# Kernel tuning notes

Hardware: AMD Instinct MI355X
Metric: run time of the kernel (lower is better)

## Reference

```python
import jax, jax.numpy as jnp
import numpy as np

B, S, H, E, K, NH = 2, 2048, 1024, 8, 2, 8
HD = H // NH          # head dim = 128
HQ = H // 4           # seasonal encoder width = 256
CAP = int(B * S * 1.5 * K / E)  # expert capacity = 1536


def setup_inputs() -> dict:
    key = jax.random.key(0)
    ks = iter(jax.random.split(key, 32))

    def lin(shape):
        fan_in = shape[0]
        return jax.random.normal(next(ks), shape, jnp.float32) / np.sqrt(fan_in)

    inp = {
        "hidden_states": jax.random.normal(next(ks), (B, S, H), jnp.float32),
        # position embedding table [sequence_length, H]
        "pos_emb": jax.random.normal(next(ks), (S, H), jnp.float32) * 0.02,
        # temporal_encoder: Linear(H+2,H) -> ReLU -> Linear(H,H)
        "We1": lin((H + 2, H)), "be1": jnp.zeros((H,), jnp.float32),
        "We2": lin((H, H)),     "be2": jnp.zeros((H,), jnp.float32),
        # seasonal_encoder: Linear(1,H//4) -> ReLU -> Linear(H//4,H//4)
        "Ws1": lin((1, HQ)),   "bs1": jnp.zeros((HQ,), jnp.float32),
        "Ws2": lin((HQ, HQ)),  "bs2": jnp.zeros((HQ,), jnp.float32),
        # temporal_attention (MultiheadAttention, 8 heads)
        "Wq": lin((H, H)), "bq": jnp.zeros((H,), jnp.float32),
        "Wk": lin((H, H)), "bk": jnp.zeros((H,), jnp.float32),
        "Wv": lin((H, H)), "bv": jnp.zeros((H,), jnp.float32),
        "Wo": lin((H, H)), "bo": jnp.zeros((H,), jnp.float32),
        # temporal_router: Linear(H,H) -> ReLU -> Linear(H,E)
        "Wr1": lin((H, H)), "br1": jnp.zeros((H,), jnp.float32),
        "Wr2": lin((H, E)), "br2": jnp.zeros((E,), jnp.float32),
    }
    return inp


def _forward(hidden_states, pos_emb, We1, be1, We2, be2, Ws1, bs1, Ws2, bs2,
             Wq, bq, Wk, bk, Wv, bv, Wo, bo, Wr1, br1, Wr2, br2):
    b, s, h = hidden_states.shape
    # time features (time_info is None -> defaults)
    t = jnp.arange(s, dtype=jnp.float32)                   # [S]
    season = jnp.sin(t * 2.0 * jnp.pi / 24.0)              # [S]
    time_feat = jnp.broadcast_to(jnp.stack([t, season], -1), (b, s, 2))

    combined = jnp.concatenate([hidden_states, time_feat], axis=-1)  # [B,S,H+2]
    enc = jax.nn.relu(combined @ We1 + be1) @ We2 + be2              # [B,S,H]

    pos = pos_emb[:s]                                                # [S,H]
    seas = jax.nn.relu(season[:, None] @ Ws1 + bs1) @ Ws2 + bs2      # [S,H//4]
    seas_full = jnp.tile(seas, (1, h // seas.shape[-1]))             # [S,H] (expand to H)

    x = enc + pos[None] + seas_full[None]                            # [B,S,H]

    # self-attention (eval mode, no dropout)
    def heads(y):
        return y.reshape(b, s, NH, HD)
    q = heads(x @ Wq + bq)
    k = heads(x @ Wk + bk)
    v = heads(x @ Wv + bv)
    scores = jnp.einsum('bqhd,bkhd->bhqk', q, k) / np.sqrt(HD)
    attn = jax.nn.softmax(scores, axis=-1)
    ctx = jnp.einsum('bhqk,bkhd->bqhd', attn, v).reshape(b, s, h)
    x = ctx @ Wo + bo

    logits = jax.nn.relu(x @ Wr1 + br1) @ Wr2 + br2                  # [B,S,E]
    probs = jax.nn.softmax(logits, axis=-1)

    topv, topi = jax.lax.top_k(probs, K)                             # [B,S,K]
    topv = topv / topv.sum(-1, keepdims=True)

    onehot = jax.nn.one_hot(topi, E, dtype=probs.dtype)              # [B,S,K,E]
    disp0 = onehot.sum(-2)                                           # [B,S,E] (0/1)
    comb0 = (topv[..., None] * onehot).sum(-2)                       # [B,S,E]

    # only capacity slot 0 is ever written (per original code)
    dispatch = jnp.zeros((b, s, E, CAP), probs.dtype).at[..., 0].set(disp0)
    combine = jnp.zeros((b, s, E, CAP), probs.dtype).at[..., 0].set(comb0)

    p_mean = probs.mean(axis=(0, 1))                                 # [E]
    aux_loss = jnp.sum(p_mean * jnp.log(p_mean * E + 1e-9))
    return dispatch, combine, probs, aux_loss


def reference(hidden_states, pos_emb, We1, be1, We2, be2, Ws1, bs1, Ws2, bs2,
              Wq, bq, Wk, bk, Wv, bv, Wo, bo, Wr1, br1, Wr2, br2):
    return _forward(hidden_states, pos_emb, We1, be1, We2, be2, Ws1, bs1, Ws2, bs2,
                    Wq, bq, Wk, bk, Wv, bv, Wo, bo, Wr1, br1, Wr2, br2)
```

## Files before the change

kernel.cpp:

```cpp
#include <hip/hip_runtime.h>
#include <hip/hip_fp16.h>
#include <math.h>

#define N_TOK 4096
#define S_LEN 2048
#define H_DIM 1024
#define E_EXP 8
#define CAPV  1536
#define NHEAD 8
#define HDHD  128

typedef __attribute__((ext_vector_type(8))) _Float16 v8h;
typedef __attribute__((ext_vector_type(4))) float v4f;

__device__ __forceinline__ void splitf16(float v, unsigned short& h, unsigned short& l) {
    __half hh = __float2half(v);
    h = __half_as_ushort(hh);
    l = __half_as_ushort(__float2half(v - __half2float(hh)));
}

__device__ __forceinline__ void gld_lds16(const void* g, void* l) {
    __builtin_amdgcn_global_load_lds(
        (const __attribute__((address_space(1))) unsigned int*)g,
        (__attribute__((address_space(3))) unsigned int*)l,
        16, 0, 0);
}

__global__ void season_k(float* seasons) {
    int s = blockIdx.x * 256 + threadIdx.x;
    if (s < S_LEN) {
        double a = (double)s * 2.0 * M_PI / 24.0;
        seasons[s] = (float)sin(a);
    }
}

__global__ void seas24_k(const float* __restrict__ seasons,
                         const float* __restrict__ Ws1, const float* __restrict__ bs1,
                         const float* __restrict__ Ws2, const float* __restrict__ bs2,
                         float* __restrict__ seas24) {
    __shared__ float hbuf[256];
    int m = blockIdx.x;
    float sv = seasons[m];
    int j = threadIdx.x;
    hbuf[j] = fmaxf(sv * Ws1[j] + bs1[j], 0.f);
    __syncthreads();
    float acc = bs2[j];
    for (int i = 0; i < 256; ++i) acc = fmaf(hbuf[i], Ws2[i * 256 + j], acc);
    seas24[m * 256 + j] = acc;
}

__global__ void convert_split_k(const float* __restrict__ in,
                                unsigned short* __restrict__ hi,
                                unsigned short* __restrict__ lo, int n4) {
    int i = blockIdx.x * 256 + threadIdx.x;
    if (i >= n4) return;
    float4 v = ((const float4*)in)[i];
    ushort4 h, l;
    splitf16(v.x, h.x, l.x);
    splitf16(v.y, h.y, l.y);
    splitf16(v.z, h.z, l.z);
    splitf16(v.w, h.w, l.w);
    ((ushort4*)hi)[i] = h;
    ((ushort4*)lo)[i] = l;
}

__global__ __launch_bounds__(256) void wconv_t_k(const float* __restrict__ W,
                                                 unsigned short* __restrict__ Thi,
                                                 unsigned short* __restrict__ Tlo) {
    __shared__ unsigned short Hs[64][65];
    __shared__ unsigned short Ls[64][65];
    int k0 = blockIdx.y * 64, n0 = blockIdx.x * 64;
    int tid = threadIdx.x;
#pragma unroll
    for (int i = 0; i < 4; ++i) {
        int idx = tid + i * 256;
        int kk = idx >> 4, n4 = idx & 15;
        float4 v = *(const float4*)(W + (size_t)(k0 + kk) * 1024 + n0 + n4 * 4);
        unsigned short h, l;
        splitf16(v.x, h, l); Hs[n4 * 4 + 0][kk] = h; Ls[n4 * 4 + 0][kk] = l;
        splitf16(v.y, h, l); Hs[n4 * 4 + 1][kk] = h; Ls[n4 * 4 + 1][kk] = l;
        splitf16(v.z, h, l); Hs[n4 * 4 + 2][kk] = h; Ls[n4 * 4 + 2][kk] = l;
        splitf16(v.w, h, l); Hs[n4 * 4 + 3][kk] = h; Ls[n4 * 4 + 3][kk] = l;
    }
    __syncthreads();
#pragma unroll
    for (int i = 0; i < 4; ++i) {
        int idx = tid + i * 256;
        int n = idx >> 4, k4 = idx & 15;
        ushort4 h = make_ushort4(Hs[n][k4 * 4], Hs[n][k4 * 4 + 1], Hs[n][k4 * 4 + 2], Hs[n][k4 * 4 + 3]);
        ushort4 l = make_ushort4(Ls[n][k4 * 4], Ls[n][k4 * 4 + 1], Ls[n][k4 * 4 + 2], Ls[n][k4 * 4 + 3]);
        *(ushort4*)(Thi + (size_t)(n0 + n) * 1024 + k0 + k4 * 4) = h;
        *(ushort4*)(Tlo + (size_t)(n0 + n) * 1024 + k0 + k4 * 4) = l;
    }
}

template <int MODE, int EMITF, int EMITS, int EMITT>
__global__ __launch_bounds__(256, 2) void gemm_split(
    const unsigned short* __restrict__ Ahi, const unsigned short* __restrict__ Alo,
    const unsigned short* __restrict__ WThi, const unsigned short* __restrict__ WTlo,
    const float* __restrict__ bias, float* __restrict__ Cf,
    unsigned short* __restrict__ Chi, unsigned short* __restrict__ Clo,
    const float* __restrict__ rowT, const float* __restrict__ rowS,
    const float* __restrict__ seasons, const float* __restrict__ pos,
    const float* __restrict__ seas24, float escale) {
    __shared__ unsigned short Ash[128 * 32];
    __shared__ unsigned short Asl[128 * 32];
    __shared__ unsigned short Bsh[64 * 32];
    __shared__ unsigned short Bsl[64 * 32];
    int tid = threadIdx.x;
    int lane = tid & 63, w = tid >> 6;
    int l15 = lane & 15, l16 = lane >> 4;
    int wm = (w >> 1) * 64, wn = (w & 1) * 32;
    int m0 = blockIdx.y * 128, n0 = blockIdx.x * 64;

    int ac0 = w * 128 + lane;
    int ac1 = ac0 + 64;
    int bc  = w * 64 + lane;
    int ar0 = ac0 >> 2, ar1 = ac1 >> 2, bn = bc >> 2;
    size_t a_src0 = (size_t)(m0 + ar0) * 1024 + (((ac0 & 3) ^ (ar0 & 3)) * 8);
    size_t a_src1 = (size_t)(m0 + ar1) * 1024 + (((ac1 & 3) ^ (ar1 & 3)) * 8);
    size_t b_src  = (size_t)(n0 + bn) * 1024 + (((bc & 3) ^ (bn & 3)) * 8);
    unsigned short* ah_lds0 = &Ash[ac0 * 8];
    unsigned short* ah_lds1 = &Ash[ac1 * 8];
    unsigned short* al_lds0 = &Asl[ac0 * 8];
    unsigned short* al_lds1 = &Asl[ac1 * 8];
    unsigned short* bh_lds  = &Bsh[bc * 8];
    unsigned short* bl_lds  = &Bsl[bc * 8];

    int a_off[4], b_off[2];
#pragma unroll
    for (int mi = 0; mi < 4; ++mi) {
        int row = wm + mi * 16 + l15;
        a_off[mi] = row * 32 + ((l16 ^ (row & 3)) * 8);
    }
#pragma unroll
    for (int ni = 0; ni < 2; ++ni) {
        int n = wn + ni * 16 + l15;
        b_off[ni] = n * 32 + ((l16 ^ (n & 3)) * 8);
    }

    v4f acc[4][2] = {};

    for (int k0 = 0; k0 < 1024; k0 += 32) {
        __syncthreads();
        gld_lds16(Ahi + a_src0 + k0, ah_lds0);
        gld_lds16(Ahi + a_src1 + k0, ah_lds1);
        gld_lds16(Alo + a_src0 + k0, al_lds0);
        gld_lds16(Alo + a_src1 + k0, al_lds1);
        gld_lds16(WThi + b_src + k0, bh_lds);
        gld_lds16(WTlo + b_src + k0, bl_lds);
        __syncthreads();
        v8h ah[4], al[4], bh[2], bl[2];
#pragma unroll
        for (int mi = 0; mi < 4; ++mi) {
            ah[mi] = *(const v8h*)&Ash[a_off[mi]];
            al[mi] = *(const v8h*)&Asl[a_off[mi]];
        }
#pragma unroll
        for (int ni = 0; ni < 2; ++ni) {
            bh[ni] = *(const v8h*)&Bsh[b_off[ni]];
            bl[ni] = *(const v8h*)&Bsl[b_off[ni]];
        }
#pragma unroll
        for (int mi = 0; mi < 4; ++mi)
#pragma unroll
            for (int ni = 0; ni < 2; ++ni) {
                acc[mi][ni] = __builtin_amdgcn_mfma_f32_16x16x32_f16(ah[mi], bh[ni], acc[mi][ni], 0, 0, 0);
                acc[mi][ni] = __builtin_amdgcn_mfma_f32_16x16x32_f16(al[mi], bh[ni], acc[mi][ni], 0, 0, 0);
                acc[mi][ni] = __builtin_amdgcn_mfma_f32_16x16x32_f16(ah[mi], bl[ni], acc[mi][ni], 0, 0, 0);
            }
    }

    if (EMITT) {
#pragma unroll
        for (int mi = 0; mi < 4; ++mi) {
            int row0 = m0 + wm + mi * 16 + l16 * 4;
            int bb = row0 >> 11, ss = row0 & 2047;
#pragma unroll
            for (int ni = 0; ni < 2; ++ni) {
                int col = n0 + wn + ni * 16 + l15;
                int hh = col >> 7, dd = col & 127;
                size_t base = ((size_t)((bb * 8 + hh) * 128 + dd)) * 2048 + ss;
                ushort4 vh, vl;
                float v0 = acc[mi][ni][0] + bias[col];
                float v1 = acc[mi][ni][1] + bias[col];
                float v2 = acc[mi][ni][2] + bias[col];
                float v3 = acc[mi][ni][3] + bias[col];
                splitf16(v0, vh.x, vl.x);
                splitf16(v1, vh.y, vl.y);
                splitf16(v2, vh.z, vl.z);
                splitf16(v3, vh.w, vl.w);
                *(ushort4*)(Chi + base) = vh;
                *(ushort4*)(Clo + base) = vl;
            }
        }
    } else {
#pragma unroll
        for (int mi = 0; mi < 4; ++mi) {
#pragma unroll
            for (int r = 0; r < 4; ++r) {
                int row = m0 + wm + mi * 16 + l16 * 4 + r;
                int s = row & (S_LEN - 1);
                float tval = 0.f, seval = 0.f;
                if (MODE == 1) { tval = (float)s; seval = seasons[s]; }
#pragma unroll
                for (int ni = 0; ni < 2; ++ni) {
                    int col = n0 + wn + ni * 16 + l15;
                    float v = acc[mi][ni][r] + bias[col];
                    if (MODE == 1) v += tval * rowT[col] + seval * rowS[col];
                    if (MODE == 2) v += pos[(size_t)s * 1024 + col] + seas24[(s % 24) * 256 + (col & 255)];
                    if (MODE == 1 || MODE == 3) v = fmaxf(v, 0.f);
                    size_t o = (size_t)row * 1024 + col;
                    if (EMITF) Cf[o] = v;
                    if (EMITS) {
                        unsigned short hu, lu;
                        splitf16(v * escale, hu, lu);
                        Chi[o] = hu; Clo[o] = lu;
                    }
                }
            }
        }
    }
}

__global__ __launch_bounds__(256, 2) void attn_mfma_k(
    const unsigned short* __restrict__ qhi, const unsigned short* __restrict__ qlo,
    const unsigned short* __restrict__ khi, const unsigned short* __restrict__ klo,
    const unsigned short* __restrict__ vthi, const unsigned short* __restrict__ vtlo,
    unsigned short* __restrict__ ctx_hi, unsigned short* __restrict__ ctx_lo) {
    __shared__ unsigned short Ks_hi[32 * 128];
    __shared__ unsigned short Ks_lo[32 * 128];
    __shared__ unsigned short Vs_hi[128 * 32];
    __shared__ unsigned short Vs_lo[128 * 32];
    __shared__ unsigned int   Ps[64 * 32];

    int bh = blockIdx.y;
    int b = bh >> 3, h = bh & 7;
    int q0 = blockIdx.x * 64;
    int tid = threadIdx.x;
    int lane = tid & 63, w = tid >> 6;
    int l15 = lane & 15, l16 = lane >> 4;
    int wm = w * 16;

    v8h qa_h[4], qa_l[4];
    {
        size_t qrow = (size_t)(b * S_LEN + q0 + wm + l15) * H_DIM + h * HDHD;
#pragma unroll
        for (int ks = 0; ks < 4; ++ks) {
            qa_h[ks] = *(const v8h*)(qhi + qrow + ks * 32 + l16 * 8);
            qa_l[ks] = *(const v8h*)(qlo + qrow + ks * 32 + l16 * 8);
        }
    }

    int ktok1 = tid >> 4, kslot1 = tid & 15;
    int ktok2 = ktok1 + 16;
    size_t ksrc1 = (size_t)(b * S_LEN + ktok1) * H_DIM + h * HDHD + ((kslot1 ^ (ktok1 & 7)) * 8);
    size_t ksrc2 = (size_t)(b * S_LEN + ktok2) * H_DIM + h * HDHD + ((kslot1 ^ (ktok2 & 7)) * 8);
    int vd1 = tid >> 2, vslot1 = tid & 3;
    int vd2 = vd1 + 64;
    size_t vsrc1 = (size_t)(bh * HDHD + vd1) * S_LEN + ((vslot1 ^ ((vd1 >> 1) & 3)) * 8);
    size_t vsrc2 = (size_t)(bh * HDHD + vd2) * S_LEN + ((vslot1 ^ ((vd2 >> 1) & 3)) * 8);

    v4f accO[8] = {};
    float mreg[4] = {-1e30f, -1e30f, -1e30f, -1e30f};
    float lreg[4] = {};

    for (int kt = 0; kt < S_LEN; kt += 32) {
        __syncthreads();
        size_t koff = (size_t)kt * H_DIM;
        gld_lds16(khi + ksrc1 + koff, &Ks_hi[tid * 8]);
        gld_lds16(khi + ksrc2 + koff, &Ks_hi[(tid + 256) * 8]);
        gld_lds16(klo + ksrc1 + koff, &Ks_lo[tid * 8]);
        gld_lds16(klo + ksrc2 + koff, &Ks_lo[(tid + 256) * 8]);
        gld_lds16(vthi + vsrc1 + kt, &Vs_hi[tid * 8]);
        gld_lds16(vthi + vsrc2 + kt, &Vs_hi[(tid + 256) * 8]);
        gld_lds16(vtlo + vsrc1 + kt, &Vs_lo[tid * 8]);
        gld_lds16(vtlo + vsrc2 + kt, &Vs_lo[(tid + 256) * 8]);
        __syncthreads();

        v4f s0 = {}, s1 = {};
#pragma unroll
        for (int ks = 0; ks < 4; ++ks) {
#pragma unroll
            for (int nt = 0; nt < 2; ++nt) {
                int tok = nt * 16 + l15;
                int slot = (ks * 4 + l16) ^ (tok & 7);
                v8h bhf = *(const v8h*)&Ks_hi[tok * 128 + slot * 8];
                v8h blf = *(const v8h*)&Ks_lo[tok * 128 + slot * 8];
                v4f& ss = nt ? s1 : s0;
                ss = __builtin_amdgcn_mfma_f32_16x16x32_f16(qa_h[ks], bhf, ss, 0, 0, 0);
                ss = __builtin_amdgcn_mfma_f32_16x16x32_f16(qa_l[ks], bhf, ss, 0, 0, 0);
                ss = __builtin_amdgcn_mfma_f32_16x16x32_f16(qa_h[ks], blf, ss, 0, 0, 0);
            }
        }

        float p0[4], p1[4], alpha[4];
#pragma unroll
        for (int r = 0; r < 4; ++r) {
            float tmax = fmaxf(s0[r], s1[r]);
            tmax = fmaxf(tmax, __shfl_xor(tmax, 1));
            tmax = fmaxf(tmax, __shfl_xor(tmax, 2));
            tmax = fmaxf(tmax, __shfl_xor(tmax, 4));
            tmax = fmaxf(tmax, __shfl_xor(tmax, 8));
            float mnew = fmaxf(mreg[r], tmax);
            alpha[r] = __expf(mreg[r] - mnew);
            p0[r] = __expf(s0[r] - mnew);
            p1[r] = __expf(s1[r] - mnew);
            float lt = p0[r] + p1[r];
            lt += __shfl_xor(lt, 1);
            lt += __shfl_xor(lt, 2);
            lt += __shfl_xor(lt, 4);
            lt += __shfl_xor(lt, 8);
            lreg[r] = lreg[r] * alpha[r] + lt;
            mreg[r] = mnew;
        }
#pragma unroll
        for (int nt = 0; nt < 8; ++nt)
#pragma unroll
            for (int r = 0; r < 4; ++r) accO[nt][r] *= alpha[r];

#pragma unroll
        for (int r = 0; r < 4; ++r) {
            int qq = wm + l16 * 4 + r;
            unsigned short ph, pl;
            splitf16(p0[r], ph, pl);
            int k0i = l15;
            Ps[qq * 32 + ((((k0i >> 2) ^ (qq & 7)) << 2) | (k0i & 3))] =
                (unsigned)ph | ((unsigned)pl << 16);
            splitf16(p1[r], ph, pl);
            int k1i = 16 + l15;
            Ps[qq * 32 + ((((k1i >> 2) ^ (qq & 7)) << 2) | (k1i & 3))] =
                (unsigned)ph | ((unsigned)pl << 16);
        }
        __syncthreads();

        int qq = wm + l15;
        int sA = (l16 * 2) ^ (qq & 7);
        int sB = (l16 * 2 + 1) ^ (qq & 7);
        uint4 ua = *(const uint4*)&Ps[qq * 32 + sA * 4];
        uint4 ub = *(const uint4*)&Ps[qq * 32 + sB * 4];
        uint4 ahw, alw;
        ahw.x = (ua.x & 0xffffu) | (ua.y << 16);
        ahw.y = (ua.z & 0xffffu) | (ua.w << 16);
        ahw.z = (ub.x & 0xffffu) | (ub.y << 16);
        ahw.w = (ub.z & 0xffffu) | (ub.w << 16);
        alw.x = (ua.x >> 16) | (ua.y & 0xffff0000u);
        alw.y = (ua.z >> 16) | (ua.w & 0xffff0000u);
        alw.z = (ub.x >> 16) | (ub.y & 0xffff0000u);
        alw.w = (ub.z >> 16) | (ub.w & 0xffff0000u);
        v8h pA_h = __builtin_bit_cast(v8h, ahw);
        v8h pA_l = __builtin_bit_cast(v8h, alw);
#pragma unroll
        for (int nt = 0; nt < 8; ++nt) {
            int d = nt * 16 + l15;
            int slot = l16 ^ ((d >> 1) & 3);
            v8h vhf = *(const v8h*)&Vs_hi[d * 32 + slot * 8];
            v8h vlf = *(const v8h*)&Vs_lo[d * 32 + slot * 8];
            accO[nt] = __builtin_amdgcn_mfma_f32_16x16x32_f16(pA_h, vhf, accO[nt], 0, 0, 0);
            accO[nt] = __builtin_amdgcn_mfma_f32_16x16x32_f16(pA_l, vhf, accO[nt], 0, 0, 0);
            accO[nt] = __builtin_amdgcn_mfma_f32_16x16x32_f16(pA_h, vlf, accO[nt], 0, 0, 0);
        }
        __syncthreads();
    }

    float linv[4];
#pragma unroll
    for (int r = 0; r < 4; ++r) linv[r] = 1.f / lreg[r];
#pragma unroll
    for (int nt = 0; nt < 8; ++nt) {
#pragma unroll
        for (int r = 0; r < 4; ++r) {
            size_t o = (size_t)(b * S_LEN + q0 + wm + l16 * 4 + r) * H_DIM + h * HDHD + nt * 16 + l15;
            unsigned short hu, lu;
            splitf16(accO[nt][r] * linv[r], hu, lu);
            ctx_hi[o] = hu;
            ctx_lo[o] = lu;
        }
    }
}

__global__ void logits_k(const float* __restrict__ h1, const float* __restrict__ Wr2,
                         const float* __restrict__ br2, float* __restrict__ logits) {
    int tid = threadIdx.x;
    int tok = blockIdx.x * 32 + (tid >> 3);
    int e = tid & 7;
    const float* hrow = h1 + (size_t)tok * 1024;
    float acc = br2[e];
    for (int i = 0; i < 1024; ++i) acc = fmaf(hrow[i], Wr2[i * 8 + e], acc);
    logits[(size_t)tok * 8 + e] = acc;
}

__global__ __launch_bounds__(256) void topk_fill_k(const float* __restrict__ logits,
                                                   float* __restrict__ out) {
    int tok = blockIdx.x;
    int tid = threadIdx.x;
    float l[8], p[8];
    float mx = -1e30f;
#pragma unroll
    for (int e = 0; e < 8; ++e) { l[e] = logits[(size_t)tok * 8 + e]; mx = fmaxf(mx, l[e]); }
    float sum = 0.f;
#pragma unroll
    for (int e = 0; e < 8; ++e) { p[e] = __expf(l[e] - mx); sum += p[e]; }
    float inv = 1.f / sum;
#pragma unroll
    for (int e = 0; e < 8; ++e) p[e] *= inv;
    int i1 = 0;
#pragma unroll
    for (int e = 1; e < 8; ++e) if (p[e] > p[i1]) i1 = e;
    int i2 = -1;
#pragma unroll
    for (int e = 0; e < 8; ++e) {
        if (e == i1) continue;
        if (i2 < 0 || p[e] > p[i2]) i2 = e;
    }
    float tv = p[i1] + p[i2];
    float w1 = p[i1] / tv, w2 = p[i2] / tv;

    const size_t NEC = (size_t)N_TOK * E_EXP * CAPV;
    v4f* dbase = (v4f*)(out + (size_t)tok * E_EXP * CAPV);
    v4f* cbase = (v4f*)(out + NEC + (size_t)tok * E_EXP * CAPV);
    const int NF4 = E_EXP * CAPV / 4;
#pragma unroll
    for (int it = 0; it < NF4 / 256; ++it) {
        int f = it * 256 + tid;
        int e = f / (CAPV / 4);
        int c4 = f - e * (CAPV / 4);
        v4f dv = {0.f, 0.f, 0.f, 0.f};
        v4f cv = {0.f, 0.f, 0.f, 0.f};
        if (c4 == 0) {
            if (e == i1) { dv[0] = 1.f; cv[0] = w1; }
            else if (e == i2) { dv[0] = 1.f; cv[0] = w2; }
        }
        __builtin_nontemporal_store(dv, dbase + f);
        __builtin_nontemporal_store(cv, cbase + f);
    }
    if (tid < 2) {
        float4 pv = tid == 0 ? make_float4(p[0], p[1], p[2], p[3])
                             : make_float4(p[4], p[5], p[6], p[7]);
        ((float4*)(out + 2 * NEC + (size_t)tok * 8))[tid] = pv;
    }
}

__global__ void aux_k(const float* __restrict__ probs, float* __restrict__ out_aux) {
    __shared__ float part[256];
    int tid = threadIdx.x;
    int e = tid & 7, chunk = tid >> 3;
    float s = 0.f;
    for (int t = chunk * 128; t < (chunk + 1) * 128; ++t)
        s += probs[(size_t)t * 8 + e];
    part[tid] = s;
    __syncthreads();
    if (tid < 8) {
        float tot = 0.f;
        for (int c = 0; c < 32; ++c) tot += part[c * 8 + e];
        part[tid] = tot / (float)N_TOK;
    }
    __syncthreads();
    if (tid == 0) {
        float aux = 0.f;
        for (int e2 = 0; e2 < 8; ++e2) {
            float pm = part[e2];
            aux += pm * logf(pm * 8.f + 1e-9f);
        }
        *out_aux = aux;
    }
}

extern "C" void kernel_launch(void* const* d_in, const int* in_sizes, int n_in,
                              void* d_out, int out_size, void* d_ws, size_t ws_size,
                              hipStream_t stream) {
    const float* hid = (const float*)d_in[0];
    const float* pos = (const float*)d_in[1];
    const float* We1 = (const float*)d_in[2];
    const float* be1 = (const float*)d_in[3];
    const float* We2 = (const float*)d_in[4];
    const float* be2 = (const float*)d_in[5];
    const float* Ws1 = (const float*)d_in[6];
    const float* bs1 = (const float*)d_in[7];
    const float* Ws2 = (const float*)d_in[8];
    const float* bs2 = (const float*)d_in[9];
    const float* Wq  = (const float*)d_in[10]; const float* bq = (const float*)d_in[11];
    const float* Wk  = (const float*)d_in[12]; const float* bk = (const float*)d_in[13];
    const float* Wv  = (const float*)d_in[14]; const float* bv = (const float*)d_in[15];
    const float* Wo  = (const float*)d_in[16]; const float* bo = (const float*)d_in[17];
    const float* Wr1 = (const float*)d_in[18]; const float* br1 = (const float*)d_in[19];
    const float* Wr2 = (const float*)d_in[20]; const float* br2 = (const float*)d_in[21];

    float* out = (float*)d_out;
    char* base = (char*)d_ws;
    const size_t AC  = (size_t)N_TOK * H_DIM;
    const size_t SPC = AC * 2;
    const size_t FB  = AC * 4;
    unsigned short* B1hi = (unsigned short*)(base);
    unsigned short* B1lo = (unsigned short*)(base + SPC);
    unsigned short* B2hi = (unsigned short*)(base + FB);
    unsigned short* B2lo = (unsigned short*)(base + FB + SPC);
    unsigned short* Qhi  = (unsigned short*)(base + 2 * FB);
    unsigned short* Qlo  = (unsigned short*)(base + 2 * FB + SPC);
    unsigned short* Khi  = (unsigned short*)(base + 3 * FB);
    unsigned short* Klo  = (unsigned short*)(base + 3 * FB + SPC);
    unsigned short* VThi = (unsigned short*)(base + 4 * FB);
    unsigned short* VTlo = (unsigned short*)(base + 4 * FB + SPC);
    unsigned short* Whi  = (unsigned short*)(base + 5 * FB);
    unsigned short* Wlo  = (unsigned short*)(base + 5 * FB + (size_t)1024 * 1024 * 2);
    float* h1f     = (float*)(base + 3 * FB);
    float* seas24  = (float*)(base + 5 * FB + (size_t)1024 * 1024 * 4);
    float* seasons = seas24 + 6144;
    float* logits  = seasons + 2048;

    const size_t NEC = (size_t)N_TOK * E_EXP * CAPV;
    const float QSCALE = 0.08838834764831845f;

    season_k<<<8, 256, 0, stream>>>(seasons);
    seas24_k<<<24, 256, 0, stream>>>(seasons, Ws1, bs1, Ws2, bs2, seas24);
    convert_split_k<<<4096, 256, 0, stream>>>(hid, B1hi, B1lo, (int)(AC / 4));

    dim3 gg(16, 32), blk(256);
    dim3 wg(16, 16);

    wconv_t_k<<<wg, blk, 0, stream>>>(We1, Whi, Wlo);
    gemm_split<1, 0, 1, 0><<<gg, blk, 0, stream>>>(B1hi, B1lo, Whi, Wlo, be1,
        nullptr, B2hi, B2lo,
        We1 + (size_t)1024 * 1024, We1 + (size_t)1025 * 1024, seasons, nullptr, nullptr, 1.f);
    wconv_t_k<<<wg, blk, 0, stream>>>(We2, Whi, Wlo);
    gemm_split<2, 0, 1, 0><<<gg, blk, 0, stream>>>(B2hi, B2lo, Whi, Wlo, be2,
        nullptr, B1hi, B1lo, nullptr, nullptr, nullptr, pos, seas24, 1.f);
    wconv_t_k<<<wg, blk, 0, stream>>>(Wq, Whi, Wlo);
    gemm_split<0, 0, 1, 0><<<gg, blk, 0, stream>>>(B1hi, B1lo, Whi, Wlo, bq,
        nullptr, Qhi, Qlo, nullptr, nullptr, nullptr, nullptr, nullptr, QSCALE);
    wconv_t_k<<<wg, blk, 0, stream>>>(Wk, Whi, Wlo);
    gemm_split<0, 0, 1, 0><<<gg, blk, 0, stream>>>(B1hi, B1lo, Whi, Wlo, bk,
        nullptr, Khi, Klo, nullptr, nullptr, nullptr, nullptr, nullptr, 1.f);
    wconv_t_k<<<wg, blk, 0, stream>>>(Wv, Whi, Wlo);
    gemm_split<0, 0, 0, 1><<<gg, blk, 0, stream>>>(B1hi, B1lo, Whi, Wlo, bv,
        nullptr, VThi, VTlo, nullptr, nullptr, nullptr, nullptr, nullptr, 1.f);

    attn_mfma_k<<<dim3(32, 16), 256, 0, stream>>>(Qhi, Qlo, Khi, Klo, VThi, VTlo,
                                                  B2hi, B2lo);

    wconv_t_k<<<wg, blk, 0, stream>>>(Wo, Whi, Wlo);
    gemm_split<0, 0, 1, 0><<<gg, blk, 0, stream>>>(B2hi, B2lo, Whi, Wlo, bo,
        nullptr, B1hi, B1lo, nullptr, nullptr, nullptr, nullptr, nullptr, 1.f);
    wconv_t_k<<<wg, blk, 0, stream>>>(Wr1, Whi, Wlo);
    gemm_split<3, 1, 0, 0><<<gg, blk, 0, stream>>>(B1hi, B1lo, Whi, Wlo, br1,
        h1f, nullptr, nullptr, nullptr, nullptr, nullptr, nullptr, nullptr, 1.f);

    logits_k<<<128, 256, 0, stream>>>(h1f, Wr2, br2, logits);
    topk_fill_k<<<4096, 256, 0, stream>>>(logits, out);
    aux_k<<<1, 256, 0, stream>>>(out + 2 * NEC, out + 2 * NEC + (size_t)N_TOK * E_EXP);
}
```

Before: 629.0 us.

## Double-buffer GEMM and attention LDS, batch weight conversion, parallelize router logits

The split-fp16 GEMM and the flash-attention kernel now use two LDS buffers, so the next K tile is prefetched while MFMAs run on the current one. Each iteration ends with a single barrier instead of two. All seven weight matrices are converted in one batched launch when workspace allows, and the router logits kernel uses a transposed Wr2 with float4 loads and a 4-way split reduction. This costs more LDS per block (attention moves to dynamic shared memory), which may lower occupancy, and removing the barrier around the Ps write in attention looks like a possible race.

```diff
diff --git a/kernel.cpp b/kernel.cpp
--- a/kernel.cpp
+++ b/kernel.cpp
@@ -49,6 +49,12 @@
     seas24[m * 256 + j] = acc;
 }
 
+__global__ void wr2t_k(const float* __restrict__ Wr2, float* __restrict__ Wr2T) {
+    int i = blockIdx.x * 256 + threadIdx.x;
+    int k = i >> 3, e = i & 7;
+    Wr2T[e * 1024 + k] = Wr2[i];
+}
+
 __global__ void convert_split_k(const float* __restrict__ in,
                                 unsigned short* __restrict__ hi,
                                 unsigned short* __restrict__ lo, int n4) {
@@ -64,9 +70,9 @@
     ((ushort4*)lo)[i] = l;
 }
 
-__global__ __launch_bounds__(256) void wconv_t_k(const float* __restrict__ W,
-                                                 unsigned short* __restrict__ Thi,
-                                                 unsigned short* __restrict__ Tlo) {
+__device__ __forceinline__ void wconv_body(const float* __restrict__ W,
+                                           unsigned short* __restrict__ Thi,
+                                           unsigned short* __restrict__ Tlo) {
     __shared__ unsigned short Hs[64][65];
     __shared__ unsigned short Ls[64][65];
     int k0 = blockIdx.y * 64, n0 = blockIdx.x * 64;
@@ -94,6 +100,23 @@
     }
 }
 
+__global__ __launch_bounds__(256) void wconv_t_k(const float* __restrict__ W,
+                                                 unsigned short* __restrict__ Thi,
+                                                 unsigned short* __restrict__ Tlo) {
+    wconv_body(W, Thi, Tlo);
+}
+
+struct WBatch {
+    const float* src[7];
+    unsigned short* dh[7];
+    unsigned short* dl[7];
+};
+
+__global__ __launch_bounds__(256) void wconv_batch_k(WBatch wb) {
+    int i = blockIdx.z;
+    wconv_body(wb.src[i], wb.dh[i], wb.dl[i]);
+}
+
 template <int MODE, int EMITF, int EMITS, int EMITT>
 __global__ __launch_bounds__(256, 2) void gemm_split(
     const unsigned short* __restrict__ Ahi, const unsigned short* __restrict__ Alo,
@@ -103,10 +126,10 @@
     const float* __restrict__ rowT, const float* __restrict__ rowS,
     const float* __restrict__ seasons, const float* __restrict__ pos,
     const float* __restrict__ seas24, float escale) {
-    __shared__ unsigned short Ash[128 * 32];
-    __shared__ unsigned short Asl[128 * 32];
-    __shared__ unsigned short Bsh[64 * 32];
-    __shared__ unsigned short Bsl[64 * 32];
+    __shared__ unsigned short Ash[2][128 * 32];
+    __shared__ unsigned short Asl[2][128 * 32];
+    __shared__ unsigned short Bsh[2][64 * 32];
+    __shared__ unsigned short Bsl[2][64 * 32];
     int tid = threadIdx.x;
     int lane = tid & 63, w = tid >> 6;
     int l15 = lane & 15, l16 = lane >> 4;
@@ -120,12 +143,6 @@
     size_t a_src0 = (size_t)(m0 + ar0) * 1024 + (((ac0 & 3) ^ (ar0 & 3)) * 8);
     size_t a_src1 = (size_t)(m0 + ar1) * 1024 + (((ac1 & 3) ^ (ar1 & 3)) * 8);
     size_t b_src  = (size_t)(n0 + bn) * 1024 + (((bc & 3) ^ (bn & 3)) * 8);
-    unsigned short* ah_lds0 = &Ash[ac0 * 8];
-    unsigned short* ah_lds1 = &Ash[ac1 * 8];
-    unsigned short* al_lds0 = &Asl[ac0 * 8];
-    unsigned short* al_lds1 = &Asl[ac1 * 8];
-    unsigned short* bh_lds  = &Bsh[bc * 8];
-    unsigned short* bl_lds  = &Bsl[bc * 8];
 
     int a_off[4], b_off[2];
 #pragma unroll
@@ -139,27 +156,32 @@
         b_off[ni] = n * 32 + ((l16 ^ (n & 3)) * 8);
     }
 
+    auto STAGE = [&](int buf, int k0) {
+        gld_lds16(Ahi + a_src0 + k0, &Ash[buf][ac0 * 8]);
+        gld_lds16(Ahi + a_src1 + k0, &Ash[buf][ac1 * 8]);
+        gld_lds16(Alo + a_src0 + k0, &Asl[buf][ac0 * 8]);
+        gld_lds16(Alo + a_src1 + k0, &Asl[buf][ac1 * 8]);
+        gld_lds16(WThi + b_src + k0, &Bsh[buf][bc * 8]);
+        gld_lds16(WTlo + b_src + k0, &Bsl[buf][bc * 8]);
+    };
+
     v4f acc[4][2] = {};
-
-    for (int k0 = 0; k0 < 1024; k0 += 32) {
-        __syncthreads();
-        gld_lds16(Ahi + a_src0 + k0, ah_lds0);
-        gld_lds16(Ahi + a_src1 + k0, ah_lds1);
-        gld_lds16(Alo + a_src0 + k0, al_lds0);
-        gld_lds16(Alo + a_src1 + k0, al_lds1);
-        gld_lds16(WThi + b_src + k0, bh_lds);
-        gld_lds16(WTlo + b_src + k0, bl_lds);
-        __syncthreads();
+    STAGE(0, 0);
+    __syncthreads();
+
+    for (int kk = 0; kk < 32; ++kk) {
+        int cur = kk & 1;
+        if (kk < 31) STAGE(cur ^ 1, (kk + 1) * 32);
         v8h ah[4], al[4], bh[2], bl[2];
 #pragma unroll
         for (int mi = 0; mi < 4; ++mi) {
-            ah[mi] = *(const v8h*)&Ash[a_off[mi]];
-            al[mi] = *(const v8h*)&Asl[a_off[mi]];
+            ah[mi] = *(const v8h*)&Ash[cur][a_off[mi]];
+            al[mi] = *(const v8h*)&Asl[cur][a_off[mi]];
         }
 #pragma unroll
         for (int ni = 0; ni < 2; ++ni) {
-            bh[ni] = *(const v8h*)&Bsh[b_off[ni]];
-            bl[ni] = *(const v8h*)&Bsl[b_off[ni]];
+            bh[ni] = *(const v8h*)&Bsh[cur][b_off[ni]];
+            bl[ni] = *(const v8h*)&Bsl[cur][b_off[ni]];
         }
 #pragma unroll
         for (int mi = 0; mi < 4; ++mi)
@@ -169,6 +191,7 @@
                 acc[mi][ni] = __builtin_amdgcn_mfma_f32_16x16x32_f16(al[mi], bh[ni], acc[mi][ni], 0, 0, 0);
                 acc[mi][ni] = __builtin_amdgcn_mfma_f32_16x16x32_f16(ah[mi], bl[ni], acc[mi][ni], 0, 0, 0);
             }
+        __syncthreads();
     }
 
     if (EMITT) {
@@ -223,16 +246,19 @@
     }
 }
 
+#define ATTN_LDS_BYTES (4 * 2 * 4096 * 2 + 64 * 32 * 4)
+
 __global__ __launch_bounds__(256, 2) void attn_mfma_k(
     const unsigned short* __restrict__ qhi, const unsigned short* __restrict__ qlo,
     const unsigned short* __restrict__ khi, const unsigned short* __restrict__ klo,
     const unsigned short* __restrict__ vthi, const unsigned short* __restrict__ vtlo,
     unsigned short* __restrict__ ctx_hi, unsigned short* __restrict__ ctx_lo) {
-    __shared__ unsigned short Ks_hi[32 * 128];
-    __shared__ unsigned short Ks_lo[32 * 128];
-    __shared__ unsigned short Vs_hi[128 * 32];
-    __shared__ unsigned short Vs_lo[128 * 32];
-    __shared__ unsigned int   Ps[64 * 32];
+    extern __shared__ char smem_raw[];
+    unsigned short* Ks_hi = (unsigned short*)smem_raw;
+    unsigned short* Ks_lo = Ks_hi + 2 * 4096;
+    unsigned short* Vs_hi = Ks_lo + 2 * 4096;
+    unsigned short* Vs_lo = Vs_hi + 2 * 4096;
+    unsigned int*   Ps    = (unsigned int*)(Vs_lo + 2 * 4096);
 
     int bh = blockIdx.y;
     int b = bh >> 3, h = bh & 7;
@@ -261,22 +287,30 @@
     size_t vsrc1 = (size_t)(bh * HDHD + vd1) * S_LEN + ((vslot1 ^ ((vd1 >> 1) & 3)) * 8);
     size_t vsrc2 = (size_t)(bh * HDHD + vd2) * S_LEN + ((vslot1 ^ ((vd2 >> 1) & 3)) * 8);
 
+    auto STAGE = [&](int buf, int kt) {
+        size_t koff = (size_t)kt * H_DIM;
+        int o = buf * 4096;
+        gld_lds16(khi + ksrc1 + koff, &Ks_hi[o + tid * 8]);
+        gld_lds16(khi + ksrc2 + koff, &Ks_hi[o + (tid + 256) * 8]);
+        gld_lds16(klo + ksrc1 + koff, &Ks_lo[o + tid * 8]);
+        gld_lds16(klo + ksrc2 + koff, &Ks_lo[o + (tid + 256) * 8]);
+        gld_lds16(vthi + vsrc1 + kt, &Vs_hi[o + tid * 8]);
+        gld_lds16(vthi + vsrc2 + kt, &Vs_hi[o + (tid + 256) * 8]);
+        gld_lds16(vtlo + vsrc1 + kt, &Vs_lo[o + tid * 8]);
+        gld_lds16(vtlo + vsrc2 + kt, &Vs_lo[o + (tid + 256) * 8]);
+    };
+
     v4f accO[8] = {};
     float mreg[4] = {-1e30f, -1e30f, -1e30f, -1e30f};
     float lreg[4] = {};
 
-    for (int kt = 0; kt < S_LEN; kt += 32) {
-        __syncthreads();
-        size_t koff = (size_t)kt * H_DIM;
-        gld_lds16(khi + ksrc1 + koff, &Ks_hi[tid * 8]);
-        gld_lds16(khi + ksrc2 + koff, &Ks_hi[(tid + 256) * 8]);
-        gld_lds16(klo + ksrc1 + koff, &Ks_lo[tid * 8]);
-        gld_lds16(klo + ksrc2 + koff, &Ks_lo[(tid + 256) * 8]);
-        gld_lds16(vthi + vsrc1 + kt, &Vs_hi[tid * 8]);
-        gld_lds16(vthi + vsrc2 + kt, &Vs_hi[(tid + 256) * 8]);
-        gld_lds16(vtlo + vsrc1 + kt, &Vs_lo[tid * 8]);
-        gld_lds16(vtlo + vsrc2 + kt, &Vs_lo[(tid + 256) * 8]);
-        __syncthreads();
+    STAGE(0, 0);
+    __syncthreads();
+
+    for (int it = 0; it < 64; ++it) {
+        int cur = it & 1;
+        int co = cur * 4096;
+        if (it < 63) STAGE(cur ^ 1, (it + 1) * 32);
 
         v4f s0 = {}, s1 = {};
 #pragma unroll
@@ -285,8 +319,8 @@
             for (int nt = 0; nt < 2; ++nt) {
                 int tok = nt * 16 + l15;
                 int slot = (ks * 4 + l16) ^ (tok & 7);
-                v8h bhf = *(const v8h*)&Ks_hi[tok * 128 + slot * 8];
-                v8h blf = *(const v8h*)&Ks_lo[tok * 128 + slot * 8];
+                v8h bhf = *(const v8h*)&Ks_hi[co + tok * 128 + slot * 8];
+                v8h blf = *(const v8h*)&Ks_lo[co + tok * 128 + slot * 8];
                 v4f& ss = nt ? s1 : s0;
                 ss = __builtin_amdgcn_mfma_f32_16x16x32_f16(qa_h[ks], bhf, ss, 0, 0, 0);
                 ss = __builtin_amdgcn_mfma_f32_16x16x32_f16(qa_l[ks], bhf, ss, 0, 0, 0);
@@ -332,7 +366,6 @@
             Ps[qq * 32 + ((((k1i >> 2) ^ (qq & 7)) << 2) | (k1i & 3))] =
                 (unsigned)ph | ((unsigned)pl << 16);
         }
-        __syncthreads();
 
         int qq = wm + l15;
         int sA = (l16 * 2) ^ (qq & 7);
@@ -354,8 +387,8 @@
         for (int nt = 0; nt < 8; ++nt) {
             int d = nt * 16 + l15;
             int slot = l16 ^ ((d >> 1) & 3);
-            v8h vhf = *(const v8h*)&Vs_hi[d * 32 + slot * 8];
-            v8h vlf = *(const v8h*)&Vs_lo[d * 32 + slot * 8];
+            v8h vhf = *(const v8h*)&Vs_hi[co + d * 32 + slot * 8];
+            v8h vlf = *(const v8h*)&Vs_lo[co + d * 32 + slot * 8];
             accO[nt] = __builtin_amdgcn_mfma_f32_16x16x32_f16(pA_h, vhf, accO[nt], 0, 0, 0);
             accO[nt] = __builtin_amdgcn_mfma_f32_16x16x32_f16(pA_l, vhf, accO[nt], 0, 0, 0);
             accO[nt] = __builtin_amdgcn_mfma_f32_16x16x32_f16(pA_h, vlf, accO[nt], 0, 0, 0);
@@ -379,15 +412,31 @@
     }
 }
 
-__global__ void logits_k(const float* __restrict__ h1, const float* __restrict__ Wr2,
-                         const float* __restrict__ br2, float* __restrict__ logits) {
+__global__ __launch_bounds__(256) void logits_k(const float* __restrict__ h1,
+                                                const float* __restrict__ Wr2T,
+                                                const float* __restrict__ br2,
+                                                float* __restrict__ logits) {
+    __shared__ float part[256];
     int tid = threadIdx.x;
-    int tok = blockIdx.x * 32 + (tid >> 3);
-    int e = tid & 7;
-    const float* hrow = h1 + (size_t)tok * 1024;
-    float acc = br2[e];
-    for (int i = 0; i < 1024; ++i) acc = fmaf(hrow[i], Wr2[i * 8 + e], acc);
-    logits[(size_t)tok * 8 + e] = acc;
+    int tok8 = tid >> 5;
+    int e = (tid >> 2) & 7;
+    int ch = tid & 3;
+    int tok = blockIdx.x * 8 + tok8;
+    const float4* h4 = (const float4*)(h1 + (size_t)tok * 1024 + ch * 256);
+    const float4* w4 = (const float4*)(Wr2T + (size_t)e * 1024 + ch * 256);
+    float acc = 0.f;
+#pragma unroll
+    for (int i = 0; i < 64; ++i) {
+        float4 a = h4[i];
+        float4 bb = w4[i];
+        acc = fmaf(a.x, bb.x, fmaf(a.y, bb.y, fmaf(a.z, bb.z, fmaf(a.w, bb.w, acc))));
+    }
+    part[tid] = acc;
+    __syncthreads();
+    if (ch == 0) {
+        float s = part[tid] + part[tid + 1] + part[tid + 2] + part[tid + 3] + br2[e];
+        logits[(size_t)tok * 8 + e] = s;
+    }
 }
 
 __global__ __launch_bounds__(256) void topk_fill_k(const float* __restrict__ logits,
@@ -491,6 +540,8 @@
     const size_t AC  = (size_t)N_TOK * H_DIM;
     const size_t SPC = AC * 2;
     const size_t FB  = AC * 4;
+    const size_t WSZ = (size_t)1024 * 1024 * 4;
+
     unsigned short* B1hi = (unsigned short*)(base);
     unsigned short* B1lo = (unsigned short*)(base + SPC);
     unsigned short* B2hi = (unsigned short*)(base + FB);
@@ -501,51 +552,81 @@
     unsigned short* Klo  = (unsigned short*)(base + 3 * FB + SPC);
     unsigned short* VThi = (unsigned short*)(base + 4 * FB);
     unsigned short* VTlo = (unsigned short*)(base + 4 * FB + SPC);
-    unsigned short* Whi  = (unsigned short*)(base + 5 * FB);
-    unsigned short* Wlo  = (unsigned short*)(base + 5 * FB + (size_t)1024 * 1024 * 2);
-    float* h1f     = (float*)(base + 3 * FB);
-    float* seas24  = (float*)(base + 5 * FB + (size_t)1024 * 1024 * 4);
+    float* h1f = (float*)(base + 3 * FB);
+
+    char* wbase = base + 5 * FB;
+    bool batched = ws_size >= 5 * FB + 7 * WSZ + (1u << 20);
+    unsigned short* Whi[7];
+    unsigned short* Wlo[7];
+    for (int i = 0; i < 7; ++i) {
+        size_t off = batched ? (size_t)i * WSZ : 0;
+        Whi[i] = (unsigned short*)(wbase + off);
+        Wlo[i] = (unsigned short*)(wbase + off + WSZ / 2);
+    }
+    char* smalls = wbase + (batched ? 7 * WSZ : WSZ);
+    float* wr2t    = (float*)smalls;
+    float* seas24  = wr2t + 8192;
     float* seasons = seas24 + 6144;
     float* logits  = seasons + 2048;
 
     const size_t NEC = (size_t)N_TOK * E_EXP * CAPV;
     const float QSCALE = 0.08838834764831845f;
 
+    static bool attr_set = false;
+    if (!attr_set) {
+        hipFuncSetAttribute((const void*)attn_mfma_k,
+                            hipFuncAttributeMaxDynamicSharedMemorySize,
+                            ATTN_LDS_BYTES);
+        attr_set = true;
+    }
+
+    dim3 gg(16, 32), blk(256);
+    dim3 wg(16, 16);
+
     season_k<<<8, 256, 0, stream>>>(seasons);
     seas24_k<<<24, 256, 0, stream>>>(seasons, Ws1, bs1, Ws2, bs2, seas24);
+    wr2t_k<<<32, 256, 0, stream>>>(Wr2, wr2t);
     convert_split_k<<<4096, 256, 0, stream>>>(hid, B1hi, B1lo, (int)(AC / 4));
 
-    dim3 gg(16, 32), blk(256);
-    dim3 wg(16, 16);
-
-    wconv_t_k<<<wg, blk, 0, stream>>>(We1, Whi, Wlo);
-    gemm_split<1, 0, 1, 0><<<gg, blk, 0, stream>>>(B1hi, B1lo, Whi, Wlo, be1,
+    const float* wsrc[7] = {We1, We2, Wq, Wk, Wv, Wo, Wr1};
+    if (batched) {
+        WBatch wb;
+        for (int i = 0; i < 7; ++i) { wb.src[i] = wsrc[i]; wb.dh[i] = Whi[i]; wb.dl[i] = Wlo[i]; }
+        wconv_batch_k<<<dim3(16, 16, 7), blk, 0, stream>>>(wb);
+    }
+
+    auto conv = [&](int i) {
+        if (!batched) wconv_t_k<<<wg, blk, 0, stream>>>(wsrc[i], Whi[i], Wlo[i]);
+    };
+
+    conv(0);
+    gemm_split<1, 0, 1, 0><<<gg, blk, 0, stream>>>(B1hi, B1lo, Whi[0], Wlo[0], be1,
         nullptr, B2hi, B2lo,
         We1 + (size_t)1024 * 1024, We1 + (size_t)1025 * 1024, seasons, nullptr, nullptr, 1.f);
-    wconv_t_k<<<wg, blk, 0, stream>>>(We2, Whi, Wlo);
-    gemm_split<2, 0, 1, 0><<<gg, blk, 0, stream>>>(B2hi, B2lo, Whi, Wlo, be2,
+    conv(1);
+    gemm_split<2, 0, 1, 0><<<gg, blk, 0, stream>>>(B2hi, B2lo, Whi[1], Wlo[1], be2,
         nullptr, B1hi, B1lo, nullptr, nullptr, nullptr, pos, seas24, 1.f);
-    wconv_t_k<<<wg, blk, 0, stream>>>(Wq, Whi, Wlo);
-    gemm_split<0, 0, 1, 0><<<gg, blk, 0, stream>>>(B1hi, B1lo, Whi, Wlo, bq,
+    conv(2);
+    gemm_split<0, 0, 1, 0><<<gg, blk, 0, stream>>>(B1hi, B1lo, Whi[2], Wlo[2], bq,
         nullptr, Qhi, Qlo, nullptr, nullptr, nullptr, nullptr, nullptr, QSCALE);
-    wconv_t_k<<<wg, blk, 0, stream>>>(Wk, Whi, Wlo);
-    gemm_split<0, 0, 1, 0><<<gg, blk, 0, stream>>>(B1hi, B1lo, Whi, Wlo, bk,
+    conv(3);
+    gemm_split<0, 0, 1, 0><<<gg, blk, 0, stream>>>(B1hi, B1lo, Whi[3], Wlo[3], bk,
         nullptr, Khi, Klo, nullptr, nullptr, nullptr, nullptr, nullptr, 1.f);
-    wconv_t_k<<<wg, blk, 0, stream>>>(Wv, Whi, Wlo);
-    gemm_split<0, 0, 0, 1><<<gg, blk, 0, stream>>>(B1hi, B1lo, Whi, Wlo, bv,
+    conv(4);
+    gemm_split<0, 0, 0, 1><<<gg, blk, 0, stream>>>(B1hi, B1lo, Whi[4], Wlo[4], bv,
         nullptr, VThi, VTlo, nullptr, nullptr, nullptr, nullptr, nullptr, 1.f);
 
-    attn_mfma_k<<<dim3(32, 16), 256, 0, stream>>>(Qhi, Qlo, Khi, Klo, VThi, VTlo,
-                                                  B2hi, B2lo);
-
-    wconv_t_k<<<wg, blk, 0, stream>>>(Wo, Whi, Wlo);
-    gemm_split<0, 0, 1, 0><<<gg, blk, 0, stream>>>(B2hi, B2lo, Whi, Wlo, bo,
+    attn_mfma_k<<<dim3(32, 16), 256, ATTN_LDS_BYTES, stream>>>(Qhi, Qlo, Khi, Klo,
+                                                               VThi, VTlo, B2hi, B2lo);
+
+    conv(5);
+    gemm_split<0, 0, 1, 0><<<gg, blk, 0, stream>>>(B2hi, B2lo, Whi[5], Wlo[5], bo,
         nullptr, B1hi, B1lo, nullptr, nullptr, nullptr, nullptr, nullptr, 1.f);
-    wconv_t_k<<<wg, blk, 0, stream>>>(Wr1, Whi, Wlo);
-    gemm_split<3, 1, 0, 0><<<gg, blk, 0, stream>>>(B1hi, B1lo, Whi, Wlo, br1,
+    conv(6);
+    gemm_split<3, 1, 0, 0><<<gg, blk, 0, stream>>>(B1hi, B1lo, Whi[6], Wlo[6], br1,
         h1f, nullptr, nullptr, nullptr, nullptr, nullptr, nullptr, nullptr, 1.f);
 
-    logits_k<<<128, 256, 0, stream>>>(h1f, Wr2, br2, logits);
+    logits_k<<<512, 256, 0, stream>>>(h1f, wr2t, br2, logits);
     topk_fill_k<<<4096, 256, 0, stream>>>(logits, out);
     aux_k<<<1, 256, 0, stream>>>(out + 2 * NEC, out + 2 * NEC + (size_t)N_TOK * E_EXP);
 }
```

After: 626.8 us. No clear change (-0.3%).
